# Kernel tuning notes

Measured on AMD Instinct MI355X. Metric: run time of the kernel, lower is better.

Reference implementation:

```python
import jax, jax.numpy as jnp
import numpy as np


def matmul_hadU(x):
    """Fast Walsh-Hadamard transform along the last dim (power of 2),
    normalized by 1/sqrt(n) — faithful translation of QuaRot's matmul_hadU
    radix-2 butterfly loop (Sylvester-ordered Hadamard)."""
    shape = x.shape
    n = shape[-1]
    assert (n & (n - 1)) == 0, "last dim must be a power of 2"
    b = x.reshape(-1, n, 1)  # (rows, m, t) with m*t == n throughout
    m, t = n, 1
    while m > 1:
        b = b.reshape(-1, m // 2, 2, t)
        lo = b[:, :, 0, :]
        hi = b[:, :, 1, :]
        b = jnp.stack([lo + hi, lo - hi], axis=2).reshape(-1, m // 2, 2 * t)
        m //= 2
        t *= 2
    scale = jnp.asarray(1.0 / np.sqrt(n), dtype=x.dtype)
    return b.reshape(shape) * scale


def setup_inputs() -> dict:
    key = jax.random.key(0)
    k1, k2, k3 = jax.random.split(key, 3)
    d = 2048
    x = jax.random.normal(k1, (4, 4096, d), dtype=jnp.float32)
    W = jax.random.normal(k2, (d, d), dtype=jnp.float32) * (1.0 / np.sqrt(d))
    b = jax.random.normal(k3, (d,), dtype=jnp.float32) * 0.01
    return {"x": x, "W": W, "b": b}


def reference(x, W, b):
    # R4Wrapper.forward: Hadamard-rotate x, then wrapped nn.Linear
    xr = matmul_hadU(x)                 # [B, S, D]
    return jnp.einsum("bsd,od->bso", xr, W) + b
```

## Files before the change

kernel.cpp:

```cpp
#include <hip/hip_runtime.h>
#include <stdint.h>

typedef __bf16 bf16x8 __attribute__((ext_vector_type(8)));
typedef float  f32x4  __attribute__((ext_vector_type(4)));
typedef unsigned short u16x8 __attribute__((ext_vector_type(8)));

__device__ __forceinline__ unsigned short f2bf(float f) {
    union { float f; unsigned int u; } v; v.f = f;
    unsigned int u = v.u;
    return (unsigned short)((u + 0x7FFFu + ((u >> 16) & 1u)) >> 16);
}

__global__ void cast_x_kernel(const float4* __restrict__ X,
                              u16x8* __restrict__ A, int n8) {
    int i = blockIdx.x * blockDim.x + threadIdx.x;
    if (i < n8) {
        float4 v0 = X[i * 2];
        float4 v1 = X[i * 2 + 1];
        u16x8 o;
        o[0] = f2bf(v0.x); o[1] = f2bf(v0.y); o[2] = f2bf(v0.z); o[3] = f2bf(v0.w);
        o[4] = f2bf(v1.x); o[5] = f2bf(v1.y); o[6] = f2bf(v1.z); o[7] = f2bf(v1.w);
        A[i] = o;
    }
}

__global__ void fwht_w_kernel(const float* __restrict__ W,
                              unsigned short* __restrict__ Bt) {
    const int n = 2048;
    __shared__ float buf[2048];
    const float* src = W + (size_t)blockIdx.x * n;
    for (int i = threadIdx.x; i < n; i += 256) buf[i] = src[i];
    __syncthreads();
    for (int len = 1; len < n; len <<= 1) {
        for (int j = threadIdx.x; j < n / 2; j += 256) {
            int idx = ((j & ~(len - 1)) << 1) | (j & (len - 1));
            float a = buf[idx], b = buf[idx + len];
            buf[idx]       = a + b;
            buf[idx + len] = a - b;
        }
        __syncthreads();
    }
    const float scale = 0.02209708691207961f;
    unsigned short* dst = Bt + (size_t)blockIdx.x * n;
    for (int i = threadIdx.x; i < n; i += 256) dst[i] = f2bf(buf[i] * scale);
}

constexpr int GK = 2048;
constexpr int GN = 2048;
constexpr int NT = GK / 32;

__global__ __launch_bounds__(512, 2) void had_gemm_kernel(
    const unsigned short* __restrict__ A,
    const unsigned short* __restrict__ B,
    const float* __restrict__ bias,
    float* __restrict__ C)
{
    __shared__ __attribute__((aligned(16))) unsigned short As[4][256 * 32];
    __shared__ __attribute__((aligned(16))) unsigned short Bs[4][256 * 32];

    const int tid  = threadIdx.x;
    const int lane = tid & 63;
    const int wave = tid >> 6;
    const int wm   = wave & 1;
    const int wn   = wave >> 1;
    const int l16  = lane & 15;
    const int quad = lane >> 4;
    const int m0 = blockIdx.y * 256;
    const int n0 = blockIdx.x * 256;

    f32x4 acc[8][4] = {};

    const int srow = tid >> 2;
    const int swzc = ((tid & 3) * 16) ^ (((srow >> 1) & 3) << 4);
    const char* gA0 = (const char*)(A + (size_t)(m0 + srow) * GK) + swzc;
    const char* gA1 = (const char*)(A + (size_t)(m0 + 128 + srow) * GK) + swzc;
    const char* gB0 = (const char*)(B + (size_t)(n0 + srow) * GK) + swzc;
    const char* gB1 = (const char*)(B + (size_t)(n0 + 128 + srow) * GK) + swzc;

#define STAGE_A(t_) { const int sl_ = (t_) & 3;                                   \
    __builtin_amdgcn_global_load_lds(                                             \
        (const __attribute__((address_space(1))) void*)(gA0 + (t_) * 64),         \
        (__attribute__((address_space(3))) void*)(&As[sl_][wave * 512]), 16, 0, 0);\
    __builtin_amdgcn_global_load_lds(                                             \
        (const __attribute__((address_space(1))) void*)(gA1 + (t_) * 64),         \
        (__attribute__((address_space(3))) void*)(&As[sl_][4096 + wave * 512]), 16, 0, 0); }
#define STAGE_B(t_) { const int sl_ = (t_) & 3;                                   \
    __builtin_amdgcn_global_load_lds(                                             \
        (const __attribute__((address_space(1))) void*)(gB0 + (t_) * 64),         \
        (__attribute__((address_space(3))) void*)(&Bs[sl_][wave * 512]), 16, 0, 0);\
    __builtin_amdgcn_global_load_lds(                                             \
        (const __attribute__((address_space(1))) void*)(gB1 + (t_) * 64),         \
        (__attribute__((address_space(3))) void*)(&Bs[sl_][4096 + wave * 512]), 16, 0, 0); }

    const int arow = wm * 128 + l16;
    const int brow = wn * 64 + l16;
    const int sw   = ((l16 >> 1) & 3) << 4;
    const unsigned aoff = (unsigned)(arow * 64 + quad * 16) ^ sw;
    const unsigned boff = (unsigned)(brow * 64 + quad * 16) ^ sw;
    const char* sabase = (const char*)&As[0][0];
    const char* sbbase = (const char*)&Bs[0][0];

    STAGE_A(0) STAGE_B(0) asm volatile("" ::: "memory");
    STAGE_A(1) STAGE_B(1) asm volatile("" ::: "memory");
    STAGE_A(2) STAGE_B(2)
    asm volatile("s_waitcnt vmcnt(8)" ::: "memory");
    __builtin_amdgcn_s_barrier();
    asm volatile("" ::: "memory");

    for (int t = 0; t < NT; ++t) {
        const char* sa = sabase + (size_t)(t & 3) * 16384;
        const char* sb = sbbase + (size_t)(t & 3) * 16384;
        bf16x8 af[8], bfr[4];

        if (t + 3 < NT) STAGE_A(t + 3);

        #pragma unroll
        for (int j = 0; j < 4; ++j)
            bfr[j] = *(const bf16x8*)(sb + (boff + j * 1024u));
        #pragma unroll
        for (int i = 0; i < 4; ++i)
            af[i] = *(const bf16x8*)(sa + (aoff + i * 1024u));

        __builtin_amdgcn_s_setprio(1);
        #pragma unroll
        for (int i = 0; i < 4; ++i)
            #pragma unroll
            for (int j = 0; j < 4; ++j)
                acc[i][j] = __builtin_amdgcn_mfma_f32_16x16x32_bf16(
                    af[i], bfr[j], acc[i][j], 0, 0, 0);
        __builtin_amdgcn_s_setprio(0);

        if (t + 3 < NT) STAGE_B(t + 3);
        #pragma unroll
        for (int i = 0; i < 4; ++i)
            af[4 + i] = *(const bf16x8*)(sa + (aoff + (4 + i) * 1024u));

        __builtin_amdgcn_s_setprio(1);
        #pragma unroll
        for (int i = 0; i < 4; ++i)
            #pragma unroll
            for (int j = 0; j < 4; ++j)
                acc[4 + i][j] = __builtin_amdgcn_mfma_f32_16x16x32_bf16(
                    af[4 + i], bfr[j], acc[4 + i][j], 0, 0, 0);
        __builtin_amdgcn_s_setprio(0);

        if (t < NT - 3)       { asm volatile("s_waitcnt vmcnt(8)" ::: "memory"); }
        else if (t == NT - 3) { asm volatile("s_waitcnt vmcnt(4)" ::: "memory"); }
        else if (t == NT - 2) { asm volatile("s_waitcnt vmcnt(0)" ::: "memory"); }
        __builtin_amdgcn_s_barrier();
        asm volatile("" ::: "memory");
    }
#undef STAGE_A
#undef STAGE_B

    float bv[4];
    #pragma unroll
    for (int j = 0; j < 4; ++j) bv[j] = bias[n0 + wn * 64 + j * 16 + l16];

    #pragma unroll
    for (int i = 0; i < 8; ++i) {
        #pragma unroll
        for (int r = 0; r < 4; ++r) {
            int row = m0 + wm * 128 + i * 16 + quad * 4 + r;
            float* cp = C + (size_t)row * GN + (n0 + wn * 64 + l16);
            #pragma unroll
            for (int j = 0; j < 4; ++j)
                cp[j * 16] = acc[i][j][r] + bv[j];
        }
    }
}

extern "C" void kernel_launch(void* const* d_in, const int* in_sizes, int n_in,
                              void* d_out, int out_size, void* d_ws, size_t ws_size,
                              hipStream_t stream) {
    const float* x = (const float*)d_in[0];
    const float* W = (const float*)d_in[1];
    const float* b = (const float*)d_in[2];
    float* out = (float*)d_out;

    const int d = in_sizes[2];
    const int M = in_sizes[0] / d;
    const int N = d, K = d;

    unsigned short* A_ws  = (unsigned short*)d_ws;
    unsigned short* Bt_ws = A_ws + (size_t)M * K;

    int n8 = in_sizes[0] / 8;
    cast_x_kernel<<<(n8 + 255) / 256, 256, 0, stream>>>(
        (const float4*)x, (u16x8*)A_ws, n8);

    fwht_w_kernel<<<N, 256, 0, stream>>>(W, Bt_ws);

    dim3 grid(N / 256, M / 256);
    had_gemm_kernel<<<grid, 512, 0, stream>>>(A_ws, Bt_ws, b, out);
}
```

Before: 394.0 us.

## Load B fragments directly from global into registers and swizzle block order

```diff
diff --git a/kernel.cpp b/kernel.cpp
--- a/kernel.cpp
+++ b/kernel.cpp
@@ -49,14 +49,13 @@
 constexpr int GN = 2048;
 constexpr int NT = GK / 32;
 
-__global__ __launch_bounds__(512, 2) void had_gemm_kernel(
+__global__ __launch_bounds__(512) void had_gemm_kernel(
     const unsigned short* __restrict__ A,
     const unsigned short* __restrict__ B,
     const float* __restrict__ bias,
     float* __restrict__ C)
 {
     __shared__ __attribute__((aligned(16))) unsigned short As[4][256 * 32];
-    __shared__ __attribute__((aligned(16))) unsigned short Bs[4][256 * 32];
 
     const int tid  = threadIdx.x;
     const int lane = tid & 63;
@@ -65,8 +64,11 @@
     const int wn   = wave >> 1;
     const int l16  = lane & 15;
     const int quad = lane >> 4;
-    const int m0 = blockIdx.y * 256;
-    const int n0 = blockIdx.x * 256;
+
+    const int lin = blockIdx.x + blockIdx.y * 8;
+    const int w   = (lin & 7) * 64 + (lin >> 3);
+    const int n0  = (w >> 6) * 256;
+    const int m0  = (w & 63) * 256;
 
     f32x4 acc[8][4] = {};
 
@@ -74,8 +76,6 @@
     const int swzc = ((tid & 3) * 16) ^ (((srow >> 1) & 3) << 4);
     const char* gA0 = (const char*)(A + (size_t)(m0 + srow) * GK) + swzc;
     const char* gA1 = (const char*)(A + (size_t)(m0 + 128 + srow) * GK) + swzc;
-    const char* gB0 = (const char*)(B + (size_t)(n0 + srow) * GK) + swzc;
-    const char* gB1 = (const char*)(B + (size_t)(n0 + 128 + srow) * GK) + swzc;
 
 #define STAGE_A(t_) { const int sl_ = (t_) & 3;                                   \
     __builtin_amdgcn_global_load_lds(                                             \
@@ -84,74 +84,71 @@
     __builtin_amdgcn_global_load_lds(                                             \
         (const __attribute__((address_space(1))) void*)(gA1 + (t_) * 64),         \
         (__attribute__((address_space(3))) void*)(&As[sl_][4096 + wave * 512]), 16, 0, 0); }
-#define STAGE_B(t_) { const int sl_ = (t_) & 3;                                   \
-    __builtin_amdgcn_global_load_lds(                                             \
-        (const __attribute__((address_space(1))) void*)(gB0 + (t_) * 64),         \
-        (__attribute__((address_space(3))) void*)(&Bs[sl_][wave * 512]), 16, 0, 0);\
-    __builtin_amdgcn_global_load_lds(                                             \
-        (const __attribute__((address_space(1))) void*)(gB1 + (t_) * 64),         \
-        (__attribute__((address_space(3))) void*)(&Bs[sl_][4096 + wave * 512]), 16, 0, 0); }
+
+    const unsigned short* gBF = B + (size_t)(n0 + wn * 64 + l16) * GK + quad * 8;
+#define LOADB(dst_, t_) {                                                         \
+    const unsigned short* p_ = gBF + (size_t)(t_) * 32;                           \
+    dst_[0] = *(const bf16x8*)(p_);                                               \
+    dst_[1] = *(const bf16x8*)(p_ + 16 * GK);                                     \
+    dst_[2] = *(const bf16x8*)(p_ + 32 * GK);                                     \
+    dst_[3] = *(const bf16x8*)(p_ + 48 * GK); }
 
     const int arow = wm * 128 + l16;
-    const int brow = wn * 64 + l16;
     const int sw   = ((l16 >> 1) & 3) << 4;
     const unsigned aoff = (unsigned)(arow * 64 + quad * 16) ^ sw;
-    const unsigned boff = (unsigned)(brow * 64 + quad * 16) ^ sw;
     const char* sabase = (const char*)&As[0][0];
-    const char* sbbase = (const char*)&Bs[0][0];
 
-    STAGE_A(0) STAGE_B(0) asm volatile("" ::: "memory");
-    STAGE_A(1) STAGE_B(1) asm volatile("" ::: "memory");
-    STAGE_A(2) STAGE_B(2)
-    asm volatile("s_waitcnt vmcnt(8)" ::: "memory");
+    bf16x8 bfrA[4], bfrB[4];
+
+    LOADB(bfrA, 0)
+    asm volatile("" ::: "memory");
+    STAGE_A(0) STAGE_A(1)
+    asm volatile("s_waitcnt vmcnt(2)" ::: "memory");
     __builtin_amdgcn_s_barrier();
     asm volatile("" ::: "memory");
 
-    for (int t = 0; t < NT; ++t) {
-        const char* sa = sabase + (size_t)(t & 3) * 16384;
-        const char* sb = sbbase + (size_t)(t & 3) * 16384;
-        bf16x8 af[8], bfr[4];
+#define TILE_BODY(t_, CUR_, NXT_) {                                               \
+    const char* sa = sabase + (size_t)((t_) & 3) * 16384;                         \
+    bf16x8 af[8];                                                                 \
+    if ((t_) + 1 < NT) { LOADB(NXT_, (t_) + 1) }                                  \
+    asm volatile("" ::: "memory");                                                \
+    if ((t_) + 2 < NT) STAGE_A((t_) + 2);                                         \
+    _Pragma("unroll")                                                             \
+    for (int i = 0; i < 4; ++i)                                                   \
+        af[i] = *(const bf16x8*)(sa + (aoff + i * 1024u));                        \
+    if ((t_) < NT - 2)       { asm volatile("s_waitcnt vmcnt(6)" ::: "memory"); } \
+    else if ((t_) == NT - 2) { asm volatile("s_waitcnt vmcnt(4)" ::: "memory"); } \
+    else                     { asm volatile("s_waitcnt vmcnt(0)" ::: "memory"); } \
+    __builtin_amdgcn_s_setprio(1);                                                \
+    _Pragma("unroll")                                                             \
+    for (int i = 0; i < 4; ++i)                                                   \
+        _Pragma("unroll")                                                         \
+        for (int j = 0; j < 4; ++j)                                               \
+            acc[i][j] = __builtin_amdgcn_mfma_f32_16x16x32_bf16(                  \
+                af[i], CUR_[j], acc[i][j], 0, 0, 0);                              \
+    __builtin_amdgcn_s_setprio(0);                                                \
+    _Pragma("unroll")                                                             \
+    for (int i = 0; i < 4; ++i)                                                   \
+        af[4 + i] = *(const bf16x8*)(sa + (aoff + (4 + i) * 1024u));              \
+    __builtin_amdgcn_s_setprio(1);                                                \
+    _Pragma("unroll")                                                             \
+    for (int i = 0; i < 4; ++i)                                                   \
+        _Pragma("unroll")                                                         \
+        for (int j = 0; j < 4; ++j)                                               \
+            acc[4 + i][j] = __builtin_amdgcn_mfma_f32_16x16x32_bf16(              \
+                af[4 + i], CUR_[j], acc[4 + i][j], 0, 0, 0);                      \
+    __builtin_amdgcn_s_setprio(0);                                                \
+    asm volatile("" ::: "memory");                                                \
+    __builtin_amdgcn_s_barrier();                                                 \
+    asm volatile("" ::: "memory"); }
 
-        if (t + 3 < NT) STAGE_A(t + 3);
-
-        #pragma unroll
-        for (int j = 0; j < 4; ++j)
-            bfr[j] = *(const bf16x8*)(sb + (boff + j * 1024u));
-        #pragma unroll
-        for (int i = 0; i < 4; ++i)
-            af[i] = *(const bf16x8*)(sa + (aoff + i * 1024u));
-
-        __builtin_amdgcn_s_setprio(1);
-        #pragma unroll
-        for (int i = 0; i < 4; ++i)
-            #pragma unroll
-            for (int j = 0; j < 4; ++j)
-                acc[i][j] = __builtin_amdgcn_mfma_f32_16x16x32_bf16(
-                    af[i], bfr[j], acc[i][j], 0, 0, 0);
-        __builtin_amdgcn_s_setprio(0);
-
-        if (t + 3 < NT) STAGE_B(t + 3);
-        #pragma unroll
-        for (int i = 0; i < 4; ++i)
-            af[4 + i] = *(const bf16x8*)(sa + (aoff + (4 + i) * 1024u));
-
-        __builtin_amdgcn_s_setprio(1);
-        #pragma unroll
-        for (int i = 0; i < 4; ++i)
-            #pragma unroll
-            for (int j = 0; j < 4; ++j)
-                acc[4 + i][j] = __builtin_amdgcn_mfma_f32_16x16x32_bf16(
-                    af[4 + i], bfr[j], acc[4 + i][j], 0, 0, 0);
-        __builtin_amdgcn_s_setprio(0);
-
-        if (t < NT - 3)       { asm volatile("s_waitcnt vmcnt(8)" ::: "memory"); }
-        else if (t == NT - 3) { asm volatile("s_waitcnt vmcnt(4)" ::: "memory"); }
-        else if (t == NT - 2) { asm volatile("s_waitcnt vmcnt(0)" ::: "memory"); }
-        __builtin_amdgcn_s_barrier();
-        asm volatile("" ::: "memory");
+    for (int t = 0; t < NT; t += 2) {
+        TILE_BODY(t,     bfrA, bfrB)
+        TILE_BODY(t + 1, bfrB, bfrA)
     }
+#undef TILE_BODY
 #undef STAGE_A
-#undef STAGE_B
+#undef LOADB
 
     float bv[4];
     #pragma unroll
```

After: 436.8 us. +10.9%, slower.
